# Kernel tuning notes

Hardware: AMD Instinct MI355X
Metric: run time of the kernel (lower is better)

The kernel has to match this reference:

```python
import jax, jax.numpy as jnp
import numpy as np

HIDDEN = 4096
INTER = 11008


def setup_inputs() -> dict:
    key = jax.random.key(0)
    k0, k1, k2, k3 = jax.random.split(key, 4)
    scale_h = 1.0 / np.sqrt(HIDDEN)
    scale_i = 1.0 / np.sqrt(INTER)
    return {
        "x": jax.random.normal(k0, (4, 32, HIDDEN), dtype=jnp.float32),
        "w_gate": jax.random.normal(k1, (INTER, HIDDEN), dtype=jnp.float32) * scale_h,
        "w_up": jax.random.normal(k2, (INTER, HIDDEN), dtype=jnp.float32) * scale_h,
        "w_down": jax.random.normal(k3, (HIDDEN, INTER), dtype=jnp.float32) * scale_i,
    }


def reference(x, w_gate, w_up, w_down):
    # SwiGLU MLP: down( silu(x @ Wg^T) * (x @ Wu^T) )
    gate = jax.nn.silu(jnp.einsum("bsh,ih->bsi", x, w_gate))
    up = jnp.einsum("bsh,ih->bsi", x, w_up)
    return jnp.einsum("bsi,hi->bsh", gate * up, w_down)
```

## Files before the change

### kernel.cpp

```cpp
#include <hip/hip_runtime.h>
#include <hip/hip_bf16.h>

#define HIDDEN 4096
#define INTER 11008
#define MTOK 128

typedef float f32x4 __attribute__((ext_vector_type(4)));
typedef short s16x8 __attribute__((ext_vector_type(8)));
typedef __attribute__((address_space(3))) unsigned int as3_u32;
typedef __attribute__((address_space(1))) unsigned int as1_u32;

__device__ __forceinline__ unsigned short f2bf(float f) {
    unsigned int u = __float_as_uint(f);
    u += 0x7FFFu + ((u >> 16) & 1u);
    return (unsigned short)(u >> 16);
}

__device__ __forceinline__ s16x8 cvt8(f32x4 a, f32x4 b) {
    s16x8 r;
    r[0] = (short)f2bf(a[0]); r[1] = (short)f2bf(a[1]);
    r[2] = (short)f2bf(a[2]); r[3] = (short)f2bf(a[3]);
    r[4] = (short)f2bf(b[0]); r[5] = (short)f2bf(b[1]);
    r[6] = (short)f2bf(b[2]); r[7] = (short)f2bf(b[3]);
    return r;
}

__global__ __launch_bounds__(256) void k_convert_x(const float* __restrict__ x,
                                                   unsigned short* __restrict__ xb) {
    int i = (blockIdx.x * 256 + threadIdx.x) * 4;
    f32x4 v = *reinterpret_cast<const f32x4*>(x + i);
    ushort4 o;
    o.x = f2bf(v[0]); o.y = f2bf(v[1]); o.z = f2bf(v[2]); o.w = f2bf(v[3]);
    *reinterpret_cast<ushort4*>(xb + i) = o;
}

template <int LDK>
__device__ __forceinline__ void gemm_body(const unsigned short* __restrict__ ab,
                                          const float* __restrict__ w, int n0,
                                          int sbeg, int send, float acc_out[8][4],
                                          unsigned short* xs, float* wlds) {
    const int tid = threadIdx.x;
    const int wv = tid >> 6, lane = tid & 63;
    const int r16 = lane & 15, g4 = lane >> 4;

    f32x4 acc[8];
#pragma unroll
    for (int i = 0; i < 8; ++i) acc[i] = (f32x4)0.0f;

    const int wrow_b = wv * 16;

    for (int s = sbeg; s < send; ++s) {
        const int k0 = s * 64;
        __syncthreads();
#pragma unroll
        for (int j = 0; j < 4; ++j) {
            int row = wrow_b + j * 4 + g4;
            const float* src = w + (size_t)(n0 + row) * LDK + k0 + (((lane & 15) ^ (row & 7)) << 2);
            __builtin_amdgcn_global_load_lds((as1_u32*)src, (as3_u32*)&wlds[(wrow_b + j * 4) * 64],
                                             16, 0, 0);
        }
#pragma unroll
        for (int i = 0; i < 4; ++i) {
            int u = tid + i * 256, row = u >> 3, off = u & 7;
            *reinterpret_cast<uint4*>(&xs[row * 72 + off * 8]) =
                *reinterpret_cast<const uint4*>(ab + (size_t)row * LDK + k0 + off * 8);
        }
        __syncthreads();
        const char* wrow = (const char*)&wlds[(wv * 16 + r16) * 64];
        const unsigned swz = (unsigned)((r16 & 7) << 4);
#pragma unroll
        for (int kk = 0; kk < 64; kk += 32) {
            f32x4 b0 = *reinterpret_cast<const f32x4*>(wrow + ((unsigned)((kk + g4 * 8) * 4) ^ swz));
            f32x4 b1 = *reinterpret_cast<const f32x4*>(wrow + ((unsigned)((kk + g4 * 8 + 4) * 4) ^ swz));
            s16x8 bf = cvt8(b0, b1);
#pragma unroll
            for (int mt = 0; mt < 8; ++mt) {
                s16x8 af = *reinterpret_cast<const s16x8*>(&xs[(mt * 16 + r16) * 72 + kk + g4 * 8]);
                acc[mt] = __builtin_amdgcn_mfma_f32_16x16x32_bf16(af, bf, acc[mt], 0, 0, 0);
            }
        }
    }
#pragma unroll
    for (int mt = 0; mt < 8; ++mt)
#pragma unroll
        for (int r = 0; r < 4; ++r) acc_out[mt][r] = acc[mt][r];
}

__global__ __launch_bounds__(256, 4) void k_gateup3(const unsigned short* __restrict__ xb,
                                                    const float* __restrict__ wg,
                                                    const float* __restrict__ wu,
                                                    float* __restrict__ pg,
                                                    float* __restrict__ pu, int Sg) {
    __shared__ __align__(16) unsigned short xs[MTOK * 72];
    __shared__ __align__(16) float wlds[64 * 64];
    const int gid = blockIdx.x;
    const int nt = gid % 172, rest = gid / 172;
    const int mat = rest & 1, kc = rest >> 1;
    const int n0 = nt * 64;
    const int nk = (HIDDEN / 64) / Sg;

    float acc[8][4];
    gemm_body<HIDDEN>(xb, mat ? wu : wg, n0, kc * nk, (kc + 1) * nk, acc, xs, wlds);

    const int lane = threadIdx.x & 63, wv = threadIdx.x >> 6;
    const int r16 = lane & 15, g4 = lane >> 4;
    float* p = (mat ? pu : pg) + (size_t)kc * (MTOK * INTER);
#pragma unroll
    for (int mt = 0; mt < 8; ++mt)
#pragma unroll
        for (int r = 0; r < 4; ++r) {
            int m = mt * 16 + g4 * 4 + r;
            p[(size_t)m * INTER + n0 + wv * 16 + r16] = acc[mt][r];
        }
}

__global__ __launch_bounds__(256) void k_combine(const float* __restrict__ pg,
                                                 const float* __restrict__ pu,
                                                 unsigned short* __restrict__ hb, int Sg) {
    size_t i = (size_t)(blockIdx.x * 256 + threadIdx.x) * 4;
    f32x4 g = (f32x4)0.0f, u = (f32x4)0.0f;
    for (int c = 0; c < Sg; ++c) {
        g += *reinterpret_cast<const f32x4*>(pg + (size_t)c * (MTOK * INTER) + i);
        u += *reinterpret_cast<const f32x4*>(pu + (size_t)c * (MTOK * INTER) + i);
    }
    ushort4 o;
    o.x = f2bf(g[0] / (1.0f + __expf(-g[0])) * u[0]);
    o.y = f2bf(g[1] / (1.0f + __expf(-g[1])) * u[1]);
    o.z = f2bf(g[2] / (1.0f + __expf(-g[2])) * u[2]);
    o.w = f2bf(g[3] / (1.0f + __expf(-g[3])) * u[3]);
    *reinterpret_cast<ushort4*>(hb + i) = o;
}

__global__ __launch_bounds__(256, 4) void k_down3(const unsigned short* __restrict__ hb,
                                                  const float* __restrict__ wd,
                                                  float* __restrict__ pd, int Sd) {
    __shared__ __align__(16) unsigned short xs[MTOK * 72];
    __shared__ __align__(16) float wlds[64 * 64];
    const int gid = blockIdx.x;
    const int nt = gid % 64, kc = gid / 64;
    const int n0 = nt * 64;
    const int sbeg = (172 * kc) / Sd, send = (172 * (kc + 1)) / Sd;

    float acc[8][4];
    gemm_body<INTER>(hb, wd, n0, sbeg, send, acc, xs, wlds);

    const int lane = threadIdx.x & 63, wv = threadIdx.x >> 6;
    const int r16 = lane & 15, g4 = lane >> 4;
    float* p = pd + (size_t)kc * (MTOK * HIDDEN);
#pragma unroll
    for (int mt = 0; mt < 8; ++mt)
#pragma unroll
        for (int r = 0; r < 4; ++r) {
            int m = mt * 16 + g4 * 4 + r;
            p[(size_t)m * HIDDEN + n0 + wv * 16 + r16] = acc[mt][r];
        }
}

__global__ __launch_bounds__(256) void k_reduce(const float* __restrict__ pd,
                                                float* __restrict__ out, int Sd) {
    int i = (blockIdx.x * 256 + threadIdx.x) * 4;
    const int NT = MTOK * HIDDEN;
    f32x4 s = (f32x4)0.0f;
    for (int c = 0; c < Sd; ++c)
        s += *reinterpret_cast<const f32x4*>(pd + (size_t)c * NT + i);
    *reinterpret_cast<f32x4*>(out + i) = s;
}

extern "C" void kernel_launch(void* const* d_in, const int* in_sizes, int n_in,
                              void* d_out, int out_size, void* d_ws, size_t ws_size,
                              hipStream_t stream) {
    const float* x  = (const float*)d_in[0];
    const float* wg = (const float*)d_in[1];
    const float* wu = (const float*)d_in[2];
    const float* wd = (const float*)d_in[3];
    float* out = (float*)d_out;

    const size_t XB = 1048576;
    const size_t HB = 2818048;
    const size_t PGU = (size_t)MTOK * INTER * 4;
    const size_t PD  = (size_t)MTOK * HIDDEN * 4;
    const int cfg[5][2] = {{4, 16}, {4, 8}, {2, 8}, {2, 4}, {1, 2}};
    int Sg = 1, Sd = 2;
    for (int c = 0; c < 5; ++c) {
        size_t need = XB + HB + 2 * (size_t)cfg[c][0] * PGU + (size_t)cfg[c][1] * PD;
        if (need <= ws_size) { Sg = cfg[c][0]; Sd = cfg[c][1]; break; }
    }

    char* ws = (char*)d_ws;
    unsigned short* xb = (unsigned short*)ws;
    unsigned short* hb = (unsigned short*)(ws + XB);
    float* pg = (float*)(ws + XB + HB);
    float* pu = pg + (size_t)Sg * (MTOK * INTER);
    float* pd = pu + (size_t)Sg * (MTOK * INTER);

    k_convert_x<<<512, 256, 0, stream>>>(x, xb);
    k_gateup3<<<172 * 2 * Sg, 256, 0, stream>>>(xb, wg, wu, pg, pu, Sg);
    k_combine<<<1376, 256, 0, stream>>>(pg, pu, hb, Sg);
    k_down3<<<64 * Sd, 256, 0, stream>>>(hb, wd, pd, Sd);
    k_reduce<<<512, 256, 0, stream>>>(pd, out, Sd);
}
```

Measured before the change: 167.4 us.

## Double-buffer weight DMA and pre-pack x into MFMA fragment layout for gate/up

The conversion kernel now writes bf16 x directly in the per-lane MFMA A-fragment order, so the gate/up kernel reads A operands straight from global memory instead of staging x through LDS. The weight tiles are double-buffered in LDS with asynchronous global-to-LDS loads for the next k-step issued before computing the current one. Each wave fetches and reads only its own weight rows, so the block-wide barriers are replaced by per-wave vmcnt waits. This aims to overlap weight streaming with MFMA work and cut LDS traffic and barrier stalls. The cost is more LDS per block, extra global traffic for the x fragments, and reliance on hand-counted vmcnt values being correct.

```diff
diff --git a/kernel.cpp b/kernel.cpp
--- a/kernel.cpp
+++ b/kernel.cpp
@@ -25,13 +25,85 @@
     return r;
 }
 
-__global__ __launch_bounds__(256) void k_convert_x(const float* __restrict__ x,
-                                                   unsigned short* __restrict__ xb) {
-    int i = (blockIdx.x * 256 + threadIdx.x) * 4;
-    f32x4 v = *reinterpret_cast<const f32x4*>(x + i);
-    ushort4 o;
-    o.x = f2bf(v[0]); o.y = f2bf(v[1]); o.z = f2bf(v[2]); o.w = f2bf(v[3]);
-    *reinterpret_cast<ushort4*>(xb + i) = o;
+__global__ __launch_bounds__(256) void k_convert_x2(const float* __restrict__ x,
+                                                    s16x8* __restrict__ xf) {
+    int t = blockIdx.x * 256 + threadIdx.x;
+    int lane = t & 63, kk2 = (t >> 6) & 1, mt = (t >> 7) & 7, s = t >> 10;
+    int row = mt * 16 + (lane & 15);
+    int k0 = s * 64 + kk2 * 32 + (lane >> 4) * 8;
+    const float* p = x + (size_t)row * HIDDEN + k0;
+    f32x4 a = *reinterpret_cast<const f32x4*>(p);
+    f32x4 b = *reinterpret_cast<const f32x4*>(p + 4);
+    xf[t] = cvt8(a, b);
+}
+
+__device__ __forceinline__ void dma_w(const float* w, int n0, int wv, int lane,
+                                      int s, float* dst) {
+    const int r16 = lane & 15, g4 = lane >> 4;
+#pragma unroll
+    for (int j = 0; j < 4; ++j) {
+        int row = wv * 16 + j * 4 + g4;
+        const float* src = w + (size_t)(n0 + row) * HIDDEN + s * 64 + ((r16 ^ (row & 7)) << 2);
+        __builtin_amdgcn_global_load_lds((as1_u32*)src,
+                                         (as3_u32*)(dst + (wv * 16 + j * 4) * 64), 16, 0, 0);
+    }
+}
+
+__global__ __launch_bounds__(256, 4) void k_gateup4(const s16x8* __restrict__ xf,
+                                                    const float* __restrict__ wg,
+                                                    const float* __restrict__ wu,
+                                                    float* __restrict__ pg,
+                                                    float* __restrict__ pu, int Sg) {
+    __shared__ __align__(16) float wlds[2][64 * 64];
+    const int tid = threadIdx.x, wv = tid >> 6, lane = tid & 63;
+    const int r16 = lane & 15, g4 = lane >> 4;
+    const int gid = blockIdx.x;
+    const int nt = gid % 172, rest = gid / 172;
+    const int mat = rest & 1, kc = rest >> 1;
+    const int n0 = nt * 64;
+    const int nk = (HIDDEN / 64) / Sg;
+    const int sbeg = kc * nk, send = (kc + 1) * nk;
+
+    const float* w = mat ? wu : wg;
+
+    f32x4 acc[8];
+#pragma unroll
+    for (int i = 0; i < 8; ++i) acc[i] = (f32x4)0.0f;
+
+    dma_w(w, n0, wv, lane, sbeg, wlds[0]);
+
+    for (int s = sbeg; s < send; ++s) {
+        const int buf = (s - sbeg) & 1;
+        if (s + 1 < send) {
+            dma_w(w, n0, wv, lane, s + 1, wlds[buf ^ 1]);
+            asm volatile("s_waitcnt vmcnt(4)" ::: "memory");
+        } else {
+            asm volatile("s_waitcnt vmcnt(0)" ::: "memory");
+        }
+        const char* wrow = (const char*)&wlds[buf][(wv * 16 + r16) * 64];
+        const unsigned swz = (unsigned)((r16 & 7) << 4);
+        const s16x8* ab = xf + (size_t)s * 1024 + lane;
+#pragma unroll
+        for (int kk2 = 0; kk2 < 2; ++kk2) {
+            f32x4 b0 = *reinterpret_cast<const f32x4*>(wrow + (((kk2 * 32 + g4 * 8) * 4) ^ swz));
+            f32x4 b1 = *reinterpret_cast<const f32x4*>(wrow + (((kk2 * 32 + g4 * 8 + 4) * 4) ^ swz));
+            s16x8 bf = cvt8(b0, b1);
+#pragma unroll
+            for (int mt = 0; mt < 8; ++mt) {
+                s16x8 af = ab[(mt * 2 + kk2) * 64];
+                acc[mt] = __builtin_amdgcn_mfma_f32_16x16x32_bf16(af, bf, acc[mt], 0, 0, 0);
+            }
+        }
+    }
+
+    float* p = (mat ? pu : pg) + (size_t)kc * (MTOK * INTER);
+#pragma unroll
+    for (int mt = 0; mt < 8; ++mt)
+#pragma unroll
+        for (int r = 0; r < 4; ++r) {
+            int m = mt * 16 + g4 * 4 + r;
+            p[(size_t)m * INTER + n0 + wv * 16 + r16] = acc[mt][r];
+        }
 }
 
 template <int LDK>
@@ -84,34 +156,6 @@
     for (int mt = 0; mt < 8; ++mt)
 #pragma unroll
         for (int r = 0; r < 4; ++r) acc_out[mt][r] = acc[mt][r];
-}
-
-__global__ __launch_bounds__(256, 4) void k_gateup3(const unsigned short* __restrict__ xb,
-                                                    const float* __restrict__ wg,
-                                                    const float* __restrict__ wu,
-                                                    float* __restrict__ pg,
-                                                    float* __restrict__ pu, int Sg) {
-    __shared__ __align__(16) unsigned short xs[MTOK * 72];
-    __shared__ __align__(16) float wlds[64 * 64];
-    const int gid = blockIdx.x;
-    const int nt = gid % 172, rest = gid / 172;
-    const int mat = rest & 1, kc = rest >> 1;
-    const int n0 = nt * 64;
-    const int nk = (HIDDEN / 64) / Sg;
-
-    float acc[8][4];
-    gemm_body<HIDDEN>(xb, mat ? wu : wg, n0, kc * nk, (kc + 1) * nk, acc, xs, wlds);
-
-    const int lane = threadIdx.x & 63, wv = threadIdx.x >> 6;
-    const int r16 = lane & 15, g4 = lane >> 4;
-    float* p = (mat ? pu : pg) + (size_t)kc * (MTOK * INTER);
-#pragma unroll
-    for (int mt = 0; mt < 8; ++mt)
-#pragma unroll
-        for (int r = 0; r < 4; ++r) {
-            int m = mt * 16 + g4 * 4 + r;
-            p[(size_t)m * INTER + n0 + wv * 16 + r16] = acc[mt][r];
-        }
 }
 
 __global__ __launch_bounds__(256) void k_combine(const float* __restrict__ pg,
@@ -187,14 +231,14 @@
     }
 
     char* ws = (char*)d_ws;
-    unsigned short* xb = (unsigned short*)ws;
+    s16x8* xf = (s16x8*)ws;
     unsigned short* hb = (unsigned short*)(ws + XB);
     float* pg = (float*)(ws + XB + HB);
     float* pu = pg + (size_t)Sg * (MTOK * INTER);
     float* pd = pu + (size_t)Sg * (MTOK * INTER);
 
-    k_convert_x<<<512, 256, 0, stream>>>(x, xb);
-    k_gateup3<<<172 * 2 * Sg, 256, 0, stream>>>(xb, wg, wu, pg, pu, Sg);
+    k_convert_x2<<<256, 256, 0, stream>>>(x, xf);
+    k_gateup4<<<172 * 2 * Sg, 256, 0, stream>>>(xf, wg, wu, pg, pu, Sg);
     k_combine<<<1376, 256, 0, stream>>>(pg, pu, hb, Sg);
     k_down3<<<64 * Sd, 256, 0, stream>>>(hb, wd, pd, Sd);
     k_reduce<<<512, 256, 0, stream>>>(pd, out, Sd);
```

New measurement: 201.7 us. 1.21x slower.

## Multi-buffer GEMM tiles with async LDS DMA and vmcnt-gated barriers

Applied to the files above, without the earlier changes.

Rewrites the shared GEMM core as a software pipeline. Weight tiles are triple-buffered and activation tiles double-buffered, both loaded by global_load_lds DMA, and each stage waits with an explicit s_waitcnt vmcnt instead of full syncthreads. The activation tile moves from padded synchronous copies to a swizzled DMA layout. Split-K factors for the down projection are halved (16→8 preferred), and occupancy bounds drop to 2 blocks per CU because LDS use grows. The aim is to overlap HBM weight streaming with MFMA work, at the cost of fewer resident blocks and less split-K parallelism.

```diff
diff --git a/kernel.cpp b/kernel.cpp
--- a/kernel.cpp
+++ b/kernel.cpp
@@ -34,73 +34,90 @@
     *reinterpret_cast<ushort4*>(xb + i) = o;
 }
 
+__device__ __forceinline__ void dma_A(const unsigned short* __restrict__ ab, int ldk,
+                                      int k0, unsigned short* abuf, int wv, int lane) {
+#pragma unroll
+    for (int j = 0; j < 4; ++j) {
+        int J = wv * 4 + j;
+        int row = J * 8 + (lane >> 3);
+        const unsigned short* src = ab + (size_t)row * ldk + k0 + 8 * ((lane & 7) ^ (lane >> 3));
+        __builtin_amdgcn_global_load_lds((as1_u32*)src, (as3_u32*)(abuf + J * 512), 16, 0, 0);
+    }
+}
+
+__device__ __forceinline__ void dma_W(const float* __restrict__ w, int ldk, int n0,
+                                      int k0, float* wbuf, int wv, int lane) {
+#pragma unroll
+    for (int j = 0; j < 4; ++j) {
+        int R = wv * 16 + j * 4;
+        int row = R + (lane >> 4);
+        const float* src = w + (size_t)(n0 + row) * ldk + k0 + 4 * ((lane & 15) ^ (row & 7));
+        __builtin_amdgcn_global_load_lds((as1_u32*)src, (as3_u32*)(wbuf + R * 64), 16, 0, 0);
+    }
+}
+
 template <int LDK>
-__device__ __forceinline__ void gemm_body(const unsigned short* __restrict__ ab,
+__device__ __forceinline__ void gemm_core(const unsigned short* __restrict__ ab,
                                           const float* __restrict__ w, int n0,
-                                          int sbeg, int send, float acc_out[8][4],
-                                          unsigned short* xs, float* wlds) {
-    const int tid = threadIdx.x;
-    const int wv = tid >> 6, lane = tid & 63;
+                                          int sbeg, int send, f32x4 acc[8],
+                                          unsigned short* alds, float* wlds) {
+    const int tid = threadIdx.x, wv = tid >> 6, lane = tid & 63;
     const int r16 = lane & 15, g4 = lane >> 4;
-
-    f32x4 acc[8];
-#pragma unroll
-    for (int i = 0; i < 8; ++i) acc[i] = (f32x4)0.0f;
-
-    const int wrow_b = wv * 16;
-
-    for (int s = sbeg; s < send; ++s) {
-        const int k0 = s * 64;
-        __syncthreads();
-#pragma unroll
-        for (int j = 0; j < 4; ++j) {
-            int row = wrow_b + j * 4 + g4;
-            const float* src = w + (size_t)(n0 + row) * LDK + k0 + (((lane & 15) ^ (row & 7)) << 2);
-            __builtin_amdgcn_global_load_lds((as1_u32*)src, (as3_u32*)&wlds[(wrow_b + j * 4) * 64],
-                                             16, 0, 0);
-        }
-#pragma unroll
-        for (int i = 0; i < 4; ++i) {
-            int u = tid + i * 256, row = u >> 3, off = u & 7;
-            *reinterpret_cast<uint4*>(&xs[row * 72 + off * 8]) =
-                *reinterpret_cast<const uint4*>(ab + (size_t)row * LDK + k0 + off * 8);
-        }
-        __syncthreads();
-        const char* wrow = (const char*)&wlds[(wv * 16 + r16) * 64];
-        const unsigned swz = (unsigned)((r16 & 7) << 4);
-#pragma unroll
-        for (int kk = 0; kk < 64; kk += 32) {
-            f32x4 b0 = *reinterpret_cast<const f32x4*>(wrow + ((unsigned)((kk + g4 * 8) * 4) ^ swz));
-            f32x4 b1 = *reinterpret_cast<const f32x4*>(wrow + ((unsigned)((kk + g4 * 8 + 4) * 4) ^ swz));
+    const int nst = send - sbeg;
+
+    dma_A(ab, LDK, sbeg * 64, alds, wv, lane);
+    dma_W(w, LDK, n0, sbeg * 64, wlds, wv, lane);
+    if (nst >= 2) dma_W(w, LDK, n0, (sbeg + 1) * 64, wlds + 4096, wv, lane);
+
+    for (int t = 0; t < nst; ++t) {
+        const int s = sbeg + t;
+        if (t + 1 < nst) dma_A(ab, LDK, (s + 1) * 64, alds + ((t + 1) & 1) * 8192, wv, lane);
+        if (t + 2 < nst) dma_W(w, LDK, n0, (s + 2) * 64, wlds + ((t + 2) % 3) * 4096, wv, lane);
+        const int rem = nst - 1 - t;
+        if (rem >= 2)      asm volatile("s_waitcnt vmcnt(12)" ::: "memory");
+        else if (rem == 1) asm volatile("s_waitcnt vmcnt(8)" ::: "memory");
+        else               asm volatile("s_waitcnt vmcnt(0)" ::: "memory");
+        __builtin_amdgcn_s_barrier();
+
+        const char* wrow = (const char*)(wlds + (t % 3) * 4096) + (wv * 16 + r16) * 256;
+        const char* arow = (const char*)(alds + (t & 1) * 8192);
+        const unsigned swz = (unsigned)(r16 & 7) << 4;
+#pragma unroll
+        for (int kk2 = 0; kk2 < 2; ++kk2) {
+            unsigned X = kk2 * 128 + g4 * 32;
+            f32x4 b0 = *reinterpret_cast<const f32x4*>(wrow + ((X) ^ swz));
+            f32x4 b1 = *reinterpret_cast<const f32x4*>(wrow + ((X + 16) ^ swz));
             s16x8 bf = cvt8(b0, b1);
+            unsigned ax = (unsigned)(kk2 * 64 + g4 * 16) ^ swz;
 #pragma unroll
             for (int mt = 0; mt < 8; ++mt) {
-                s16x8 af = *reinterpret_cast<const s16x8*>(&xs[(mt * 16 + r16) * 72 + kk + g4 * 8]);
+                s16x8 af = *reinterpret_cast<const s16x8*>(arow + (mt * 16 + r16) * 128 + ax);
                 acc[mt] = __builtin_amdgcn_mfma_f32_16x16x32_bf16(af, bf, acc[mt], 0, 0, 0);
             }
         }
-    }
-#pragma unroll
-    for (int mt = 0; mt < 8; ++mt)
-#pragma unroll
-        for (int r = 0; r < 4; ++r) acc_out[mt][r] = acc[mt][r];
-}
-
-__global__ __launch_bounds__(256, 4) void k_gateup3(const unsigned short* __restrict__ xb,
+        __builtin_amdgcn_s_barrier();
+    }
+}
+
+__global__ __launch_bounds__(256, 2) void k_gateup6(const unsigned short* __restrict__ xb,
                                                     const float* __restrict__ wg,
                                                     const float* __restrict__ wu,
                                                     float* __restrict__ pg,
                                                     float* __restrict__ pu, int Sg) {
-    __shared__ __align__(16) unsigned short xs[MTOK * 72];
-    __shared__ __align__(16) float wlds[64 * 64];
+    __shared__ __align__(16) float wlds[3 * 64 * 64];
+    __shared__ __align__(16) unsigned short alds[2 * 128 * 64];
     const int gid = blockIdx.x;
     const int nt = gid % 172, rest = gid / 172;
     const int mat = rest & 1, kc = rest >> 1;
     const int n0 = nt * 64;
-    const int nk = (HIDDEN / 64) / Sg;
-
-    float acc[8][4];
-    gemm_body<HIDDEN>(xb, mat ? wu : wg, n0, kc * nk, (kc + 1) * nk, acc, xs, wlds);
+    const int nsteps = 64 / Sg;
+    const int sbeg = kc * nsteps, send = sbeg + nsteps;
+
+    f32x4 acc[8];
+#pragma unroll
+    for (int i = 0; i < 8; ++i) acc[i] = (f32x4)0.0f;
+
+    gemm_core<HIDDEN>(xb, mat ? wu : wg, n0, sbeg, send, acc, alds, wlds);
 
     const int lane = threadIdx.x & 63, wv = threadIdx.x >> 6;
     const int r16 = lane & 15, g4 = lane >> 4;
@@ -131,18 +148,21 @@
     *reinterpret_cast<ushort4*>(hb + i) = o;
 }
 
-__global__ __launch_bounds__(256, 4) void k_down3(const unsigned short* __restrict__ hb,
+__global__ __launch_bounds__(256, 2) void k_down6(const unsigned short* __restrict__ hb,
                                                   const float* __restrict__ wd,
                                                   float* __restrict__ pd, int Sd) {
-    __shared__ __align__(16) unsigned short xs[MTOK * 72];
-    __shared__ __align__(16) float wlds[64 * 64];
+    __shared__ __align__(16) float wlds[3 * 64 * 64];
+    __shared__ __align__(16) unsigned short alds[2 * 128 * 64];
     const int gid = blockIdx.x;
     const int nt = gid % 64, kc = gid / 64;
     const int n0 = nt * 64;
     const int sbeg = (172 * kc) / Sd, send = (172 * (kc + 1)) / Sd;
 
-    float acc[8][4];
-    gemm_body<INTER>(hb, wd, n0, sbeg, send, acc, xs, wlds);
+    f32x4 acc[8];
+#pragma unroll
+    for (int i = 0; i < 8; ++i) acc[i] = (f32x4)0.0f;
+
+    gemm_core<INTER>(hb, wd, n0, sbeg, send, acc, alds, wlds);
 
     const int lane = threadIdx.x & 63, wv = threadIdx.x >> 6;
     const int r16 = lane & 15, g4 = lane >> 4;
@@ -179,9 +199,9 @@
     const size_t HB = 2818048;
     const size_t PGU = (size_t)MTOK * INTER * 4;
     const size_t PD  = (size_t)MTOK * HIDDEN * 4;
-    const int cfg[5][2] = {{4, 16}, {4, 8}, {2, 8}, {2, 4}, {1, 2}};
-    int Sg = 1, Sd = 2;
-    for (int c = 0; c < 5; ++c) {
+    const int cfg[4][2] = {{4, 8}, {2, 4}, {1, 2}, {1, 1}};
+    int Sg = 1, Sd = 1;
+    for (int c = 0; c < 4; ++c) {
         size_t need = XB + HB + 2 * (size_t)cfg[c][0] * PGU + (size_t)cfg[c][1] * PD;
         if (need <= ws_size) { Sg = cfg[c][0]; Sd = cfg[c][1]; break; }
     }
@@ -194,8 +214,8 @@
     float* pd = pu + (size_t)Sg * (MTOK * INTER);
 
     k_convert_x<<<512, 256, 0, stream>>>(x, xb);
-    k_gateup3<<<172 * 2 * Sg, 256, 0, stream>>>(xb, wg, wu, pg, pu, Sg);
+    k_gateup6<<<172 * 2 * Sg, 256, 0, stream>>>(xb, wg, wu, pg, pu, Sg);
     k_combine<<<1376, 256, 0, stream>>>(pg, pu, hb, Sg);
-    k_down3<<<64 * Sd, 256, 0, stream>>>(hb, wd, pd, Sd);
+    k_down6<<<64 * Sd, 256, 0, stream>>>(hb, wd, pd, Sd);
     k_reduce<<<512, 256, 0, stream>>>(pd, out, Sd);
 }
```

Measured after the change: 178.6 us. 1.07x slower.
